# Optimization experiments

Hardware: AMD Instinct MI355X
Metric: run time of the kernel (lower is better)

Reference implementation:

```python
import jax, jax.numpy as jnp
import numpy as np

GROUPS = 8
EPS = 1e-3  # Keras GroupNormalization default epsilon


def group_norm(x, gamma, beta):
    b, h, w, c = x.shape
    xr = x.reshape(b, h, w, GROUPS, c // GROUPS)
    mean = jnp.mean(xr, axis=(1, 2, 4), keepdims=True)
    var = jnp.var(xr, axis=(1, 2, 4), keepdims=True)
    xn = ((xr - mean) * jax.lax.rsqrt(var + EPS)).reshape(b, h, w, c)
    return xn * gamma + beta


def setup_inputs() -> dict:
    key = jax.random.key(0)
    ks = jax.random.split(key, 6)
    B, H, W, C = 4, 64, 64, 256
    std = C ** -0.5
    return {
        "x": jax.random.normal(ks[0], (B, H, W, C), dtype=jnp.float32),
        "gamma": jnp.ones((C,), jnp.float32),
        "beta": jnp.zeros((C,), jnp.float32),
        "wq": jax.random.normal(ks[1], (C, C), jnp.float32) * std,
        "bq": jnp.zeros((C,), jnp.float32),
        "wk": jax.random.normal(ks[2], (C, C), jnp.float32) * std,
        "bk": jnp.zeros((C,), jnp.float32),
        "wv": jax.random.normal(ks[3], (C, C), jnp.float32) * std,
        "bv": jnp.zeros((C,), jnp.float32),
        "wp": jax.random.normal(ks[4], (C, C), jnp.float32) * std,
        "bp": jnp.zeros((C,), jnp.float32),
    }


def reference(x, gamma, beta, wq, bq, wk, bk, wv, bv, wp, bp):
    b, h, w, c = x.shape
    scale = jnp.asarray(c, x.dtype) ** -0.5
    xn = group_norm(x, gamma, beta)
    # 1x1 convs are per-pixel dense layers
    q = (xn @ wq + bq).reshape(b, h * w, c)
    k = (xn @ wk + bk).reshape(b, h * w, c)
    v = (xn @ wv + bv).reshape(b, h * w, c)
    scores = jnp.einsum('bic,bjc->bij', q, k) * scale  # [b, N, N]
    attn = jax.nn.softmax(scores, axis=-1)
    out = jnp.einsum('bij,bjc->bic', attn, v).reshape(b, h, w, c)
    return x + (out @ wp + bp)
```

## Files before the change

### kernel.cpp

```cpp
#include <hip/hip_runtime.h>

#define N_TOK 4096
#define C_DIM 256
#define BATCH 4
#define M_ROWS (BATCH * N_TOK)
#define GN_CNT 131072.0f
#define JSPLIT 4

typedef __attribute__((ext_vector_type(4))) float f32x4;
typedef __attribute__((ext_vector_type(16))) float f32x16;
typedef __attribute__((ext_vector_type(8))) short s16x8;
typedef __attribute__((ext_vector_type(4))) unsigned short u16x4;
typedef __attribute__((ext_vector_type(4))) unsigned int u32x4;

static __device__ __forceinline__ unsigned short f2bf(float f) {
  unsigned int u = __builtin_bit_cast(unsigned int, f);
  u += 0x7fff + ((u >> 16) & 1);
  return (unsigned short)(u >> 16);
}
static __device__ __forceinline__ float bf2f(unsigned short h) {
  unsigned int u = ((unsigned int)h) << 16;
  return __builtin_bit_cast(float, u);
}

static __device__ __forceinline__ void gload_lds16(const void* g, void* l) {
  __builtin_amdgcn_global_load_lds(
      (__attribute__((address_space(1))) void*)(unsigned long long)(const char*)g,
      (__attribute__((address_space(3))) void*)l, 16, 0, 0);
}

__global__ __launch_bounds__(256) void wtrans(const float* __restrict__ wq,
                                              const float* __restrict__ wk,
                                              const float* __restrict__ wv,
                                              const float* __restrict__ wp,
                                              unsigned short* __restrict__ wT) {
  const float* const srcs[4] = {wq, wk, wv, wp};
  const float* w = srcs[blockIdx.z];
  unsigned short* o = wT + blockIdx.z * 65536;
  __shared__ float t[32][33];
  int k0 = blockIdx.x * 32, n0 = blockIdx.y * 32;
  int tx = threadIdx.x, ty = threadIdx.y;
#pragma unroll
  for (int ky = 0; ky < 32; ky += 8)
    t[ty + ky][tx] = w[(k0 + ty + ky) * C_DIM + n0 + tx];
  __syncthreads();
#pragma unroll
  for (int ky = 0; ky < 32; ky += 8)
    o[(n0 + ty + ky) * C_DIM + k0 + tx] = f2bf(t[tx][ty + ky]);
}

__global__ __launch_bounds__(256) void gn_stats(const float* __restrict__ x,
                                                float* __restrict__ partials) {
  int bg = blockIdx.x >> 4, chunk = blockIdx.x & 15;
  int b = bg >> 3, g = bg & 7;
  int tid = threadIdx.x;
  const f32x4* x4 = (const f32x4*)x;
  float s1 = 0.f, s2 = 0.f;
#pragma unroll
  for (int it = 0; it < 8; ++it) {
    int idx = it * 256 + tid;
    int nl = idx >> 3, cq = idx & 7;
    f32x4 v = x4[(b * N_TOK + chunk * 256 + nl) * 64 + g * 8 + cq];
    s1 += v[0] + v[1] + v[2] + v[3];
    s2 += v[0] * v[0] + v[1] * v[1] + v[2] * v[2] + v[3] * v[3];
  }
  for (int m = 1; m < 64; m <<= 1) {
    s1 += __shfl_xor(s1, m, 64);
    s2 += __shfl_xor(s2, m, 64);
  }
  __shared__ float r1[4], r2[4];
  int wave = tid >> 6, lane = tid & 63;
  if (lane == 0) { r1[wave] = s1; r2[wave] = s2; }
  __syncthreads();
  if (tid == 0) {
    atomicAdd(&partials[bg * 2],     r1[0] + r1[1] + r1[2] + r1[3]);
    atomicAdd(&partials[bg * 2 + 1], r2[0] + r2[1] + r2[2] + r2[3]);
  }
}

__global__ __launch_bounds__(256) void gn_norm(const float* __restrict__ x,
                                               const float* __restrict__ gamma,
                                               const float* __restrict__ beta,
                                               const float* __restrict__ partials,
                                               unsigned short* __restrict__ xn) {
  const f32x4* x4 = (const f32x4*)x;
  const f32x4* g4 = (const f32x4*)gamma;
  const f32x4* b4 = (const f32x4*)beta;
  u16x4* o4 = (u16x4*)xn;
  int t0 = blockIdx.x * 256 + threadIdx.x;
#pragma unroll
  for (int it = 0; it < 4; ++it) {
    int fid = it * 262144 + t0;
    int row = fid >> 6, c4 = fid & 63;
    int b = row >> 12, g = c4 >> 3;
    int bg = b * 8 + g;
    float inv = 1.f / GN_CNT;
    float mean = partials[bg * 2] * inv;
    float var = partials[bg * 2 + 1] * inv - mean * mean;
    float rstd = rsqrtf(var + 1e-3f);
    f32x4 v = x4[fid], ga = g4[c4], be = b4[c4];
    u16x4 o;
#pragma unroll
    for (int j = 0; j < 4; ++j) o[j] = f2bf((v[j] - mean) * rstd * ga[j] + be[j]);
    o4[fid] = o;
  }
}

__global__ __launch_bounds__(256) void qkv_gemm(const unsigned short* __restrict__ xn,
                                                const unsigned short* __restrict__ wT,
                                                const float* __restrict__ bq,
                                                const float* __restrict__ bk,
                                                const float* __restrict__ bv,
                                                unsigned short* __restrict__ qo,
                                                unsigned short* __restrict__ ko,
                                                unsigned short* __restrict__ vo) {
  int tid = threadIdx.x;
  int wave = tid >> 6, lane = tid & 63, g = lane >> 4, c16 = lane & 15;
  int row0 = blockIdx.x * 64 + wave * 16;
  int w = blockIdx.y;
  s16x8 af[8];
#pragma unroll
  for (int s = 0; s < 8; ++s)
    af[s] = *(const s16x8*)(xn + (row0 + c16) * C_DIM + s * 32 + g * 8);
  const float* bias = (w == 0) ? bq : (w == 1) ? bk : bv;
  unsigned short* outp = (w == 0) ? qo : (w == 1) ? ko : vo;
  float scale = (w == 0) ? 0.0625f : 1.f;
  const unsigned short* wt = wT + w * 65536;
  for (int ct = 0; ct < 16; ++ct) {
    float bv0 = bias[ct * 16 + c16];
    f32x4 acc = {bv0, bv0, bv0, bv0};
#pragma unroll
    for (int s = 0; s < 8; ++s) {
      s16x8 bf = *(const s16x8*)(wt + (ct * 16 + c16) * C_DIM + s * 32 + g * 8);
      acc = __builtin_amdgcn_mfma_f32_16x16x32_bf16(af[s], bf, acc, 0, 0, 0);
    }
#pragma unroll
    for (int r = 0; r < 4; ++r)
      outp[(row0 + g * 4 + r) * C_DIM + ct * 16 + c16] = f2bf(acc[r] * scale);
  }
}

__global__ __launch_bounds__(256) void vtrans(const unsigned short* __restrict__ v,
                                              unsigned short* __restrict__ vT) {
  __shared__ unsigned short t[32][33];
  int n0 = blockIdx.x * 32, c0 = blockIdx.y * 32, b = blockIdx.z;
  int tx = threadIdx.x, ty = threadIdx.y;
#pragma unroll
  for (int ky = 0; ky < 32; ky += 8)
    t[ty + ky][tx] = v[(b * N_TOK + n0 + ty + ky) * C_DIM + c0 + tx];
  __syncthreads();
#pragma unroll
  for (int ky = 0; ky < 32; ky += 8)
    vT[(b * C_DIM + c0 + ty + ky) * N_TOK + n0 + tx] = t[tx][ty + ky];
}

__global__ __launch_bounds__(256, 2) void attn_part(const unsigned short* __restrict__ q,
                                                    const unsigned short* __restrict__ k,
                                                    const unsigned short* __restrict__ vT,
                                                    unsigned short* __restrict__ op0,
                                                    unsigned short* __restrict__ op1,
                                                    unsigned short* __restrict__ op2,
                                                    unsigned short* __restrict__ op3,
                                                    float* __restrict__ lbuf) {
  int tid = threadIdx.x;
  int wave = tid >> 6, lane = tid & 63;
  int n32 = lane & 31, half = lane >> 5;
  int i = blockIdx.x;
  int batch = (i >> 1) & 3;
  int slot = ((i >> 3) << 1) | (i & 1);
  int qb = slot & 31, chunk = slot >> 5;
  int qrow0 = batch * N_TOK + qb * 128 + wave * 32;
  const unsigned short* kb = k + (size_t)batch * N_TOK * C_DIM;
  const unsigned short* vb = vT + (size_t)batch * C_DIM * N_TOK;
  unsigned short* op = (chunk == 0) ? op0 : (chunk == 1) ? op1 : (chunk == 2) ? op2 : op3;

  __shared__ __align__(16) unsigned short Kt[2][8192];
  __shared__ __align__(16) unsigned short Vt[2][8192];

  const unsigned short* qp = q + (size_t)(qrow0 + n32) * C_DIM;
  s16x8 qf[16];
#pragma unroll
  for (int ks = 0; ks < 16; ++ks)
    qf[ks] = *(const s16x8*)(qp + ks * 16 + half * 8);

  f32x16 Oa[8];
#pragma unroll
  for (int ct = 0; ct < 8; ++ct) Oa[ct] = (f32x16)(0.f);
  float ls = 0.f;
  int swz = n32 & 7;

  {
    int jbase = chunk * 1024;
#pragma unroll
    for (int ii = 0; ii < 4; ++ii) {
      int u = ii * 256 + tid;
      int tok = u >> 5, un = u & 31;
      gload_lds16(kb + (size_t)(jbase + tok) * C_DIM + ((un ^ (tok & 7)) * 8), &Kt[0][u * 8]);
    }
#pragma unroll
    for (int ii = 0; ii < 4; ++ii) {
      gload_lds16(vb + (size_t)tid * N_TOK + jbase + ii * 8, &Vt[0][(ii * 256 + tid) * 8]);
    }
  }

  int cur = 0;
  for (int jt = 0; jt < 32; ++jt) {
    __syncthreads();
    if (jt < 31) {
      int jbase = chunk * 1024 + (jt + 1) * 32;
      int nxt = cur ^ 1;
#pragma unroll
      for (int ii = 0; ii < 4; ++ii) {
        int u = ii * 256 + tid;
        int tok = u >> 5, un = u & 31;
        gload_lds16(kb + (size_t)(jbase + tok) * C_DIM + ((un ^ (tok & 7)) * 8), &Kt[nxt][u * 8]);
      }
#pragma unroll
      for (int ii = 0; ii < 4; ++ii) {
        gload_lds16(vb + (size_t)tid * N_TOK + jbase + ii * 8, &Vt[nxt][(ii * 256 + tid) * 8]);
      }
    }
    const unsigned short* KT = Kt[cur];
    const unsigned short* VT = Vt[cur];

    f32x16 sc = (f32x16)(0.f);
#pragma unroll
    for (int ks = 0; ks < 16; ++ks) {
      s16x8 kf = *(const s16x8*)(KT + n32 * 256 + (((ks * 2 + half) ^ swz) * 8));
      sc = __builtin_amdgcn_mfma_f32_32x32x16_bf16(kf, qf[ks], sc, 0, 0, 0);
    }
    unsigned D[8];
#pragma unroll
    for (int t = 0; t < 8; ++t) {
      float pa = exp2f(fmaf(sc[2 * t],     1.44269504f, -11.54156032f));
      float pb = exp2f(fmaf(sc[2 * t + 1], 1.44269504f, -11.54156032f));
      ls += pa + pb;
      D[t] = (unsigned)f2bf(pa) | ((unsigned)f2bf(pb) << 16);
    }
    unsigned E[8];
#pragma unroll
    for (int t = 0; t < 8; ++t) E[t] = __shfl_xor(D[t], 32);
    u32x4 w0 = {half ? E[2] : D[0], half ? E[3] : D[1],
                half ? D[2] : E[0], half ? D[3] : E[1]};
    u32x4 w1 = {half ? E[6] : D[4], half ? E[7] : D[5],
                half ? D[6] : E[4], half ? D[7] : E[5]};
    s16x8 pf0 = __builtin_bit_cast(s16x8, w0);
    s16x8 pf1 = __builtin_bit_cast(s16x8, w1);
#pragma unroll
    for (int ct = 0; ct < 8; ++ct) {
      int ch = ct * 32 + n32;
      s16x8 vf0 = *(const s16x8*)(VT + (half * 256 + ch) * 8);
      s16x8 vf1 = *(const s16x8*)(VT + ((2 + half) * 256 + ch) * 8);
      Oa[ct] = __builtin_amdgcn_mfma_f32_32x32x16_bf16(pf0, vf0, Oa[ct], 0, 0, 0);
      Oa[ct] = __builtin_amdgcn_mfma_f32_32x32x16_bf16(pf1, vf1, Oa[ct], 0, 0, 0);
    }
    cur ^= 1;
  }
#pragma unroll
  for (int ct = 0; ct < 8; ++ct)
#pragma unroll
    for (int r = 0; r < 16; ++r) {
      int row = (r & 3) + 8 * (r >> 2) + 4 * half;
      op[(size_t)(qrow0 + row) * C_DIM + ct * 32 + n32] = f2bf(Oa[ct][r]);
    }
  float tot = ls + __shfl_xor(ls, 32);
  if (half == 0) lbuf[chunk * M_ROWS + qrow0 + n32] = tot;
}

__global__ __launch_bounds__(256) void proj_gemm(const unsigned short* __restrict__ p0,
                                                 const unsigned short* __restrict__ p1,
                                                 const unsigned short* __restrict__ p2,
                                                 const unsigned short* __restrict__ p3,
                                                 const float* __restrict__ lbuf,
                                                 const unsigned short* __restrict__ wt,
                                                 const float* __restrict__ bp,
                                                 const float* __restrict__ x,
                                                 float* __restrict__ out) {
  int tid = threadIdx.x;
  int wave = tid >> 6, lane = tid & 63, g = lane >> 4, c16 = lane & 15;
  int row0 = blockIdx.x * 64 + wave * 16;
  int ct0 = blockIdx.y * 8;
  int row = row0 + c16;
  float linv = 1.f / (lbuf[row] + lbuf[M_ROWS + row] +
                      lbuf[2 * M_ROWS + row] + lbuf[3 * M_ROWS + row]);
  s16x8 af[8];
#pragma unroll
  for (int s = 0; s < 8; ++s) {
    size_t off = (size_t)row * C_DIM + s * 32 + g * 8;
    s16x8 a0 = *(const s16x8*)(p0 + off);
    s16x8 a1 = *(const s16x8*)(p1 + off);
    s16x8 a2 = *(const s16x8*)(p2 + off);
    s16x8 a3 = *(const s16x8*)(p3 + off);
    s16x8 o;
#pragma unroll
    for (int j = 0; j < 8; ++j) {
      float f = bf2f((unsigned short)a0[j]) + bf2f((unsigned short)a1[j]) +
                bf2f((unsigned short)a2[j]) + bf2f((unsigned short)a3[j]);
      o[j] = (short)f2bf(f * linv);
    }
    af[s] = o;
  }
  for (int ct = ct0; ct < ct0 + 8; ++ct) {
    float bias = bp[ct * 16 + c16];
    f32x4 acc = {bias, bias, bias, bias};
#pragma unroll
    for (int s = 0; s < 8; ++s) {
      s16x8 bf = *(const s16x8*)(wt + (ct * 16 + c16) * C_DIM + s * 32 + g * 8);
      acc = __builtin_amdgcn_mfma_f32_16x16x32_bf16(af[s], bf, acc, 0, 0, 0);
    }
#pragma unroll
    for (int r = 0; r < 4; ++r) {
      int idx = (row0 + g * 4 + r) * C_DIM + ct * 16 + c16;
      out[idx] = acc[r] + x[idx];
    }
  }
}

extern "C" void kernel_launch(void* const* d_in, const int* in_sizes, int n_in,
                              void* d_out, int out_size, void* d_ws, size_t ws_size,
                              hipStream_t stream) {
  const float* x     = (const float*)d_in[0];
  const float* gamma = (const float*)d_in[1];
  const float* beta  = (const float*)d_in[2];
  const float* wq    = (const float*)d_in[3];
  const float* bq    = (const float*)d_in[4];
  const float* wk    = (const float*)d_in[5];
  const float* bk    = (const float*)d_in[6];
  const float* wv    = (const float*)d_in[7];
  const float* bv    = (const float*)d_in[8];
  const float* wp    = (const float*)d_in[9];
  const float* bp    = (const float*)d_in[10];
  float* out = (float*)d_out;

  char* ws = (char*)d_ws;
  const size_t MC = (size_t)M_ROWS * C_DIM;
  float* partials      = (float*)ws;
  unsigned short* wT   = (unsigned short*)(ws + 1024);
  unsigned short* xnb  = wT + 4 * 65536;
  unsigned short* qb   = xnb + MC;
  unsigned short* kbuf = qb + MC;
  unsigned short* vb   = kbuf + MC;
  unsigned short* vTb  = vb + MC;
  unsigned short* exA  = vTb + MC;
  unsigned short* exB  = exA + MC;
  float* lbuf          = (float*)(exB + MC);
  unsigned short* plane0 = xnb;
  unsigned short* plane1 = vb;

  hipMemsetAsync(partials, 0, 64 * sizeof(float), stream);
  wtrans<<<dim3(8, 8, 4), dim3(32, 8), 0, stream>>>(wq, wk, wv, wp, wT);
  gn_stats<<<512, 256, 0, stream>>>(x, partials);
  gn_norm<<<1024, 256, 0, stream>>>(x, gamma, beta, partials, xnb);
  qkv_gemm<<<dim3(256, 3), 256, 0, stream>>>(xnb, wT, bq, bk, bv, qb, kbuf, vb);
  vtrans<<<dim3(128, 8, 4), dim3(32, 8), 0, stream>>>(vb, vTb);
  attn_part<<<512, 256, 0, stream>>>(qb, kbuf, vTb, plane0, plane1, exA, exB, lbuf);
  proj_gemm<<<dim3(256, 2), 256, 0, stream>>>(plane0, plane1, exA, exB, lbuf,
                                              wT + 3 * 65536, bp, x, out);
}
```

Measured before the change: 265.3 us.

## Fuse group-norm normalize into QKV GEMM and retile GEMMs with LDS-staged weights

Removes the separate gn_norm kernel. The QKV GEMM now reads fp32 x directly and applies the group-norm mean/rstd, gamma and beta in registers before the MFMA, which avoids writing and re-reading a bf16 normalized buffer. Both the QKV and projection GEMMs switch to 32x32x16 MFMA tiles over 128 rows by 128 columns. The weight slice is staged into swizzled LDS through direct global-to-LDS loads, with launch bounds asking for two blocks per CU. The trade-off is 64KB of LDS per block, and each column-half block recomputes the normalization.

```diff
diff --git a/kernel.cpp b/kernel.cpp
--- a/kernel.cpp
+++ b/kernel.cpp
@@ -78,65 +78,81 @@
   }
 }
 
-__global__ __launch_bounds__(256) void gn_norm(const float* __restrict__ x,
-                                               const float* __restrict__ gamma,
-                                               const float* __restrict__ beta,
-                                               const float* __restrict__ partials,
-                                               unsigned short* __restrict__ xn) {
-  const f32x4* x4 = (const f32x4*)x;
-  const f32x4* g4 = (const f32x4*)gamma;
-  const f32x4* b4 = (const f32x4*)beta;
-  u16x4* o4 = (u16x4*)xn;
-  int t0 = blockIdx.x * 256 + threadIdx.x;
-#pragma unroll
-  for (int it = 0; it < 4; ++it) {
-    int fid = it * 262144 + t0;
-    int row = fid >> 6, c4 = fid & 63;
-    int b = row >> 12, g = c4 >> 3;
-    int bg = b * 8 + g;
-    float inv = 1.f / GN_CNT;
-    float mean = partials[bg * 2] * inv;
-    float var = partials[bg * 2 + 1] * inv - mean * mean;
-    float rstd = rsqrtf(var + 1e-3f);
-    f32x4 v = x4[fid], ga = g4[c4], be = b4[c4];
-    u16x4 o;
-#pragma unroll
-    for (int j = 0; j < 4; ++j) o[j] = f2bf((v[j] - mean) * rstd * ga[j] + be[j]);
-    o4[fid] = o;
-  }
-}
-
-__global__ __launch_bounds__(256) void qkv_gemm(const unsigned short* __restrict__ xn,
-                                                const unsigned short* __restrict__ wT,
-                                                const float* __restrict__ bq,
-                                                const float* __restrict__ bk,
-                                                const float* __restrict__ bv,
-                                                unsigned short* __restrict__ qo,
-                                                unsigned short* __restrict__ ko,
-                                                unsigned short* __restrict__ vo) {
+__global__ __launch_bounds__(256, 2) void qkv_gemm(const float* __restrict__ x,
+                                                   const unsigned short* __restrict__ wT,
+                                                   const float* __restrict__ partials,
+                                                   const float* __restrict__ gamma,
+                                                   const float* __restrict__ beta,
+                                                   const float* __restrict__ bq,
+                                                   const float* __restrict__ bk,
+                                                   const float* __restrict__ bv,
+                                                   unsigned short* __restrict__ qo,
+                                                   unsigned short* __restrict__ ko,
+                                                   unsigned short* __restrict__ vo) {
   int tid = threadIdx.x;
-  int wave = tid >> 6, lane = tid & 63, g = lane >> 4, c16 = lane & 15;
-  int row0 = blockIdx.x * 64 + wave * 16;
-  int w = blockIdx.y;
-  s16x8 af[8];
-#pragma unroll
-  for (int s = 0; s < 8; ++s)
-    af[s] = *(const s16x8*)(xn + (row0 + c16) * C_DIM + s * 32 + g * 8);
+  int wave = tid >> 6, lane = tid & 63, n32 = lane & 31, half = lane >> 5;
+  int row0 = blockIdx.x * 128 + wave * 32;
+  int w = blockIdx.y >> 1;
+  int c0 = (blockIdx.y & 1) * 128;
+  const unsigned short* wt = wT + w * 65536;
+  __shared__ __align__(16) unsigned short Wt[32768];
+
+#pragma unroll
+  for (int ii = 0; ii < 32; ++ii) {
+    int u = ii * 256 + tid;
+    int n = u >> 5, ku = u & 31;
+    gload_lds16(wt + (size_t)(c0 + n) * C_DIM + ((ku ^ (n & 7)) * 8), Wt + u * 8);
+  }
+
+  int row = row0 + n32;
+  int batch = row >> 12;
+  float mean[8], rstd[8];
+  float inv = 1.f / GN_CNT;
+#pragma unroll
+  for (int g = 0; g < 8; ++g) {
+    float m = partials[(batch * 8 + g) * 2] * inv;
+    float v = partials[(batch * 8 + g) * 2 + 1] * inv - m * m;
+    mean[g] = m;
+    rstd[g] = rsqrtf(v + 1e-3f);
+  }
+  s16x8 af[16];
+#pragma unroll
+  for (int ks = 0; ks < 16; ++ks) {
+    int cb = ks * 16 + half * 8;
+    const f32x4* xp = (const f32x4*)(x + (size_t)row * C_DIM + cb);
+    f32x4 v0 = xp[0], v1 = xp[1];
+    const f32x4* g4 = (const f32x4*)(gamma + cb);
+    const f32x4* b4 = (const f32x4*)(beta + cb);
+    f32x4 ga0 = g4[0], ga1 = g4[1], be0 = b4[0], be1 = b4[1];
+    int g = (2 * ks + half) >> 2;
+    float m = mean[g], rs = rstd[g];
+    s16x8 o;
+#pragma unroll
+    for (int j = 0; j < 4; ++j) {
+      o[j]     = (short)f2bf((v0[j] - m) * rs * ga0[j] + be0[j]);
+      o[4 + j] = (short)f2bf((v1[j] - m) * rs * ga1[j] + be1[j]);
+    }
+    af[ks] = o;
+  }
   const float* bias = (w == 0) ? bq : (w == 1) ? bk : bv;
   unsigned short* outp = (w == 0) ? qo : (w == 1) ? ko : vo;
   float scale = (w == 0) ? 0.0625f : 1.f;
-  const unsigned short* wt = wT + w * 65536;
-  for (int ct = 0; ct < 16; ++ct) {
-    float bv0 = bias[ct * 16 + c16];
-    f32x4 acc = {bv0, bv0, bv0, bv0};
-#pragma unroll
-    for (int s = 0; s < 8; ++s) {
-      s16x8 bf = *(const s16x8*)(wt + (ct * 16 + c16) * C_DIM + s * 32 + g * 8);
-      acc = __builtin_amdgcn_mfma_f32_16x16x32_bf16(af[s], bf, acc, 0, 0, 0);
-    }
-#pragma unroll
-    for (int r = 0; r < 4; ++r)
-      outp[(row0 + g * 4 + r) * C_DIM + ct * 16 + c16] = f2bf(acc[r] * scale);
+  __syncthreads();
+
+#pragma unroll
+  for (int ct = 0; ct < 4; ++ct) {
+    int nl = ct * 32 + n32;
+    f32x16 acc = (f32x16)(bias[c0 + nl]);
+#pragma unroll
+    for (int ks = 0; ks < 16; ++ks) {
+      s16x8 wf = *(const s16x8*)(Wt + nl * C_DIM + (((2 * ks + half) ^ (nl & 7)) * 8));
+      acc = __builtin_amdgcn_mfma_f32_32x32x16_bf16(af[ks], wf, acc, 0, 0, 0);
+    }
+#pragma unroll
+    for (int r = 0; r < 16; ++r) {
+      int rr = (r & 3) + 8 * (r >> 2) + 4 * half;
+      outp[(size_t)(row0 + rr) * C_DIM + c0 + nl] = f2bf(acc[r] * scale);
+    }
   }
 }
 
@@ -267,26 +283,35 @@
   if (half == 0) lbuf[chunk * M_ROWS + qrow0 + n32] = tot;
 }
 
-__global__ __launch_bounds__(256) void proj_gemm(const unsigned short* __restrict__ p0,
-                                                 const unsigned short* __restrict__ p1,
-                                                 const unsigned short* __restrict__ p2,
-                                                 const unsigned short* __restrict__ p3,
-                                                 const float* __restrict__ lbuf,
-                                                 const unsigned short* __restrict__ wt,
-                                                 const float* __restrict__ bp,
-                                                 const float* __restrict__ x,
-                                                 float* __restrict__ out) {
+__global__ __launch_bounds__(256, 2) void proj_gemm(const unsigned short* __restrict__ p0,
+                                                    const unsigned short* __restrict__ p1,
+                                                    const unsigned short* __restrict__ p2,
+                                                    const unsigned short* __restrict__ p3,
+                                                    const float* __restrict__ lbuf,
+                                                    const unsigned short* __restrict__ wt,
+                                                    const float* __restrict__ bp,
+                                                    const float* __restrict__ x,
+                                                    float* __restrict__ out) {
   int tid = threadIdx.x;
-  int wave = tid >> 6, lane = tid & 63, g = lane >> 4, c16 = lane & 15;
-  int row0 = blockIdx.x * 64 + wave * 16;
-  int ct0 = blockIdx.y * 8;
-  int row = row0 + c16;
+  int wave = tid >> 6, lane = tid & 63, n32 = lane & 31, half = lane >> 5;
+  int row0 = blockIdx.x * 128 + wave * 32;
+  int c0 = blockIdx.y * 128;
+  __shared__ __align__(16) unsigned short Wt[32768];
+
+#pragma unroll
+  for (int ii = 0; ii < 32; ++ii) {
+    int u = ii * 256 + tid;
+    int n = u >> 5, ku = u & 31;
+    gload_lds16(wt + (size_t)(c0 + n) * C_DIM + ((ku ^ (n & 7)) * 8), Wt + u * 8);
+  }
+
+  int row = row0 + n32;
   float linv = 1.f / (lbuf[row] + lbuf[M_ROWS + row] +
                       lbuf[2 * M_ROWS + row] + lbuf[3 * M_ROWS + row]);
-  s16x8 af[8];
-#pragma unroll
-  for (int s = 0; s < 8; ++s) {
-    size_t off = (size_t)row * C_DIM + s * 32 + g * 8;
+  s16x8 af[16];
+#pragma unroll
+  for (int ks = 0; ks < 16; ++ks) {
+    size_t off = (size_t)row * C_DIM + ks * 16 + half * 8;
     s16x8 a0 = *(const s16x8*)(p0 + off);
     s16x8 a1 = *(const s16x8*)(p1 + off);
     s16x8 a2 = *(const s16x8*)(p2 + off);
@@ -298,19 +323,23 @@
                 bf2f((unsigned short)a2[j]) + bf2f((unsigned short)a3[j]);
       o[j] = (short)f2bf(f * linv);
     }
-    af[s] = o;
-  }
-  for (int ct = ct0; ct < ct0 + 8; ++ct) {
-    float bias = bp[ct * 16 + c16];
-    f32x4 acc = {bias, bias, bias, bias};
-#pragma unroll
-    for (int s = 0; s < 8; ++s) {
-      s16x8 bf = *(const s16x8*)(wt + (ct * 16 + c16) * C_DIM + s * 32 + g * 8);
-      acc = __builtin_amdgcn_mfma_f32_16x16x32_bf16(af[s], bf, acc, 0, 0, 0);
-    }
-#pragma unroll
-    for (int r = 0; r < 4; ++r) {
-      int idx = (row0 + g * 4 + r) * C_DIM + ct * 16 + c16;
+    af[ks] = o;
+  }
+  __syncthreads();
+
+#pragma unroll
+  for (int ct = 0; ct < 4; ++ct) {
+    int nl = ct * 32 + n32;
+    f32x16 acc = (f32x16)(bp[c0 + nl]);
+#pragma unroll
+    for (int ks = 0; ks < 16; ++ks) {
+      s16x8 wf = *(const s16x8*)(Wt + nl * C_DIM + (((2 * ks + half) ^ (nl & 7)) * 8));
+      acc = __builtin_amdgcn_mfma_f32_32x32x16_bf16(af[ks], wf, acc, 0, 0, 0);
+    }
+#pragma unroll
+    for (int r = 0; r < 16; ++r) {
+      int rr = (r & 3) + 8 * (r >> 2) + 4 * half;
+      size_t idx = (size_t)(row0 + rr) * C_DIM + c0 + nl;
       out[idx] = acc[r] + x[idx];
     }
   }
@@ -336,24 +365,23 @@
   const size_t MC = (size_t)M_ROWS * C_DIM;
   float* partials      = (float*)ws;
   unsigned short* wT   = (unsigned short*)(ws + 1024);
-  unsigned short* xnb  = wT + 4 * 65536;
-  unsigned short* qb   = xnb + MC;
+  unsigned short* qb   = wT + 4 * 65536;
   unsigned short* kbuf = qb + MC;
   unsigned short* vb   = kbuf + MC;
   unsigned short* vTb  = vb + MC;
-  unsigned short* exA  = vTb + MC;
-  unsigned short* exB  = exA + MC;
-  float* lbuf          = (float*)(exB + MC);
-  unsigned short* plane0 = xnb;
-  unsigned short* plane1 = vb;
+  unsigned short* pl0  = vTb + MC;
+  unsigned short* pl2  = pl0 + MC;
+  unsigned short* pl3  = pl2 + MC;
+  float* lbuf          = (float*)(pl3 + MC);
+  unsigned short* pl1  = vb;
 
   hipMemsetAsync(partials, 0, 64 * sizeof(float), stream);
   wtrans<<<dim3(8, 8, 4), dim3(32, 8), 0, stream>>>(wq, wk, wv, wp, wT);
   gn_stats<<<512, 256, 0, stream>>>(x, partials);
-  gn_norm<<<1024, 256, 0, stream>>>(x, gamma, beta, partials, xnb);
-  qkv_gemm<<<dim3(256, 3), 256, 0, stream>>>(xnb, wT, bq, bk, bv, qb, kbuf, vb);
+  qkv_gemm<<<dim3(128, 6), 256, 0, stream>>>(x, wT, partials, gamma, beta,
+                                             bq, bk, bv, qb, kbuf, vb);
   vtrans<<<dim3(128, 8, 4), dim3(32, 8), 0, stream>>>(vb, vTb);
-  attn_part<<<512, 256, 0, stream>>>(qb, kbuf, vTb, plane0, plane1, exA, exB, lbuf);
-  proj_gemm<<<dim3(256, 2), 256, 0, stream>>>(plane0, plane1, exA, exB, lbuf,
+  attn_part<<<512, 256, 0, stream>>>(qb, kbuf, vTb, pl0, pl1, pl2, pl3, lbuf);
+  proj_gemm<<<dim3(128, 2), 256, 0, stream>>>(pl0, pl1, pl2, pl3, lbuf,
                                               wT + 3 * 65536, bp, x, out);
 }
```

After: 230.6 us. 1.15x faster.
